# Kernel tuning notes

Measured on AMD Instinct MI355X. Metric: run time of the kernel, lower is better.

Reference implementation:

```python
import jax, jax.numpy as jnp
import numpy as np

DISCOUNT_FACTOR = 0.99
ADVANTAGE_LAMBDA = 0.95
LAMBD_GRAD_SCALE = 0.5


def setup_inputs() -> dict:
    key = jax.random.key(0)
    k1, k2, k3 = jax.random.split(key, 3)
    B, T, D = 4096, 2048, 1
    values = jax.random.normal(k1, (B, T + 1, D), dtype=jnp.float32)
    rewards = jax.random.normal(k2, (B, T, D), dtype=jnp.float32)
    # binary terminal flags (float, as in the torch module: used as (1 - dones))
    dones = (jax.random.uniform(k3, (B, T, D)) < 0.02).astype(jnp.float32)
    raw_gamma = jnp.zeros((1,), dtype=jnp.float32)
    raw_lambd = jnp.zeros((T,), dtype=jnp.float32)
    return {
        "values": values,
        "rewards": rewards,
        "dones": dones,
        "raw_gamma": raw_gamma,
        "raw_lambd": raw_lambd,
        "start_idx": 0,
        "end_idx": T,
    }


def reference(values, rewards, dones, raw_gamma, raw_lambd, start_idx, end_idx):
    # dynamic gamma / lambda (sigmoid-reparameterized around the base values)
    gamma = DISCOUNT_FACTOR + (1.0 - DISCOUNT_FACTOR) * (2.0 * jax.nn.sigmoid(raw_gamma) - 1.0)
    dyn_lambd = ADVANTAGE_LAMBDA + (1.0 - ADVANTAGE_LAMBDA) * (2.0 * jax.nn.sigmoid(raw_lambd) - 1.0)
    # GradScaler(scale=0.5): forward identity, gradient scaled by 0.5
    lambd = LAMBD_GRAD_SCALE * dyn_lambd + jax.lax.stop_gradient((1.0 - LAMBD_GRAD_SCALE) * dyn_lambd)
    g = gamma[0]
    td_l = lambd[start_idx:end_idx]                      # [T]

    # time-major views for the reverse-time scan
    r_tm = jnp.moveaxis(rewards, 1, 0)                   # [T, B, D]
    d_tm = jnp.moveaxis(dones, 1, 0)                     # [T, B, D]
    vn_tm = jnp.moveaxis(values[:, 1:, :], 1, 0)         # [T, B, D] = values[t+1]

    def step(carry, x):
        sum_r, lam_ret = carry
        r, d, vn, l = x
        cont = g * (1.0 - d)
        # torch computes sum_rewards under no_grad -> stop_gradient here
        new_sum = jax.lax.stop_gradient(r + cont * (l * sum_r))
        new_lam = r + cont * ((1.0 - l) * vn + l * lam_ret)
        return (new_sum, new_lam), (new_sum, new_lam)

    init = (jnp.zeros_like(values[:, -1, :]), values[:, -1, :])
    _, (sums_tm, lams_tm) = jax.lax.scan(step, init, (r_tm, d_tm, vn_tm, td_l), reverse=True)

    lambda_returns = jnp.concatenate(
        [jnp.moveaxis(lams_tm, 0, 1), values[:, -1:, :]], axis=1
    )                                                    # [B, T+1, D]
    sum_rewards = jnp.moveaxis(sums_tm, 0, 1)            # [B, T, D] (== torch sum_rewards[:, :-1])
    return lambda_returns, sum_rewards
```

## Files before the change

### kernel.cpp

```cpp
#include <hip/hip_runtime.h>


#define TPB 256
#define EPT 8

typedef float v4f __attribute__((ext_vector_type(4)));

struct Aff { float aL, aS, b; };

__device__ inline Aff compose(const Aff& L, const Aff& R) {
    Aff o;
    o.aL = fmaf(L.b, R.aL, L.aL);
    o.aS = fmaf(L.b, R.aS, L.aS);
    o.b  = L.b * R.b;
    return o;
}

__global__ void precompute_kernel(const float* __restrict__ raw_gamma,
                                  const float* __restrict__ raw_lambd,
                                  const int* __restrict__ start_p,
                                  float* __restrict__ lam, int T) {
    int t = blockIdx.x * blockDim.x + threadIdx.x;
    if (t < T) lam[t] = 0.9f + 0.1f / (1.0f + __expf(-raw_lambd[start_p[0] + t]));
    if (t == 0) lam[T] = 0.98f + 0.02f / (1.0f + __expf(-raw_gamma[0]));
}

__global__ __launch_bounds__(TPB, 8)
void td_scan_kernel(const float* __restrict__ values,
                    const float* __restrict__ rewards,
                    const float* __restrict__ dones,
                    const float* __restrict__ lam_arr,
                    float* __restrict__ out,
                    int B, int T)
{
    __shared__ __align__(16) float s_buf[2064];
    __shared__ float s_wAL[4], s_wAS[4], s_wB[4], s_cL[4], s_cS[4];

    const int b    = blockIdx.x;
    const int tid  = threadIdx.x;
    const int lane = tid & 63;
    const int wave = tid >> 6;
    const int nwaves = TPB >> 6;

    const float g = lam_arr[T];

    const size_t rowV = (size_t)b * (T + 1);
    const float* rrow = rewards + (size_t)b * T;
    const float* drow = dones   + (size_t)b * T;

    const size_t firstNeeded = rowV + 1;
    const int off = (int)(firstNeeded & 3);
    const size_t A = firstNeeded - off;
    const int nStage = T + off;
    const int n4 = (nStage + 3) >> 2;
    const size_t totalElems = (size_t)B * (T + 1);
    for (int j = tid; j < n4; j += TPB) {
        const size_t gb = A + 4 * (size_t)j;
        if (gb + 3 < totalElems) {
            *(v4f*)(s_buf + 4 * j) = *(const v4f*)(values + gb);
        } else {
            #pragma unroll
            for (int c = 0; c < 4; ++c)
                s_buf[4 * j + c] = (gb + c < totalElems) ? values[gb + c] : 0.0f;
        }
    }
    __syncthreads();

    const float vT = s_buf[off + T - 1];

    const int base = tid * EPT;
    float r[EPT], d[EPT], l[EPT], vn[EPT];
    {
        const v4f r0 = *(const v4f*)(rrow + base);
        const v4f r1 = *(const v4f*)(rrow + base + 4);
        const v4f d0 = *(const v4f*)(drow + base);
        const v4f d1 = *(const v4f*)(drow + base + 4);
        const v4f l0 = *(const v4f*)(lam_arr + base);
        const v4f l1 = *(const v4f*)(lam_arr + base + 4);
        r[0]=r0.x; r[1]=r0.y; r[2]=r0.z; r[3]=r0.w; r[4]=r1.x; r[5]=r1.y; r[6]=r1.z; r[7]=r1.w;
        d[0]=d0.x; d[1]=d0.y; d[2]=d0.z; d[3]=d0.w; d[4]=d1.x; d[5]=d1.y; d[6]=d1.z; d[7]=d1.w;
        l[0]=l0.x; l[1]=l0.y; l[2]=l0.z; l[3]=l0.w; l[4]=l1.x; l[5]=l1.y; l[6]=l1.z; l[7]=l1.w;
    }
    {
        const v4f w0 = *(const v4f*)(s_buf + base);
        const v4f w1 = *(const v4f*)(s_buf + base + 4);
        const v4f w2 = *(const v4f*)(s_buf + base + 8);
        switch (off) {
        case 0: vn[0]=w0.x; vn[1]=w0.y; vn[2]=w0.z; vn[3]=w0.w; vn[4]=w1.x; vn[5]=w1.y; vn[6]=w1.z; vn[7]=w1.w; break;
        case 1: vn[0]=w0.y; vn[1]=w0.z; vn[2]=w0.w; vn[3]=w1.x; vn[4]=w1.y; vn[5]=w1.z; vn[6]=w1.w; vn[7]=w2.x; break;
        case 2: vn[0]=w0.z; vn[1]=w0.w; vn[2]=w1.x; vn[3]=w1.y; vn[4]=w1.z; vn[5]=w1.w; vn[6]=w2.x; vn[7]=w2.y; break;
        default: vn[0]=w0.w; vn[1]=w1.x; vn[2]=w1.y; vn[3]=w1.z; vn[4]=w1.w; vn[5]=w2.x; vn[6]=w2.y; vn[7]=w2.z; break;
        }
    }

    Aff M[EPT];
    #pragma unroll
    for (int k = 0; k < EPT; ++k) {
        const float cont = g * (1.0f - d[k]);
        M[k].b  = cont * l[k];
        M[k].aL = fmaf(cont * (1.0f - l[k]), vn[k], r[k]);
        M[k].aS = r[k];
    }
    Aff C = M[EPT - 1];
    #pragma unroll
    for (int k = EPT - 2; k >= 0; --k) C = compose(M[k], C);

    Aff S = C;
    #pragma unroll
    for (int dlt = 1; dlt < 64; dlt <<= 1) {
        Aff oth;
        oth.aL = __shfl_down(S.aL, dlt, 64);
        oth.aS = __shfl_down(S.aS, dlt, 64);
        oth.b  = __shfl_down(S.b,  dlt, 64);
        if (lane + dlt < 64) S = compose(S, oth);
    }
    Aff E;
    E.aL = __shfl_down(S.aL, 1, 64);
    E.aS = __shfl_down(S.aS, 1, 64);
    E.b  = __shfl_down(S.b,  1, 64);
    if (lane == 63) { E.aL = 0.0f; E.aS = 0.0f; E.b = 1.0f; }

    if (lane == 0) { s_wAL[wave] = S.aL; s_wAS[wave] = S.aS; s_wB[wave] = S.b; }
    __syncthreads();

    if (tid == 0) {
        float cL = vT, cS = 0.0f;
        for (int w = nwaves - 1; w >= 0; --w) {
            s_cL[w] = cL; s_cS[w] = cS;
            const float wb = s_wB[w];
            cL = fmaf(wb, cL, s_wAL[w]);
            cS = fmaf(wb, cS, s_wAS[w]);
        }
    }
    __syncthreads();

    const float cwL = s_cL[wave];
    const float cwS = s_cS[wave];
    float xL = fmaf(E.b, cwL, E.aL);
    float xS = fmaf(E.b, cwS, E.aS);
    float oL[EPT], oS[EPT];
    #pragma unroll
    for (int k = EPT - 1; k >= 0; --k) {
        xL = fmaf(M[k].b, xL, M[k].aL);
        xS = fmaf(M[k].b, xS, M[k].aS);
        oL[k] = xL; oS[k] = xS;
    }

    float* sum_out = out + (size_t)B * (T + 1) + (size_t)b * T;
    {
        v4f s0 = { oS[0], oS[1], oS[2], oS[3] };
        v4f s1 = { oS[4], oS[5], oS[6], oS[7] };
        __builtin_nontemporal_store(s0, (v4f*)(sum_out + base));
        __builtin_nontemporal_store(s1, (v4f*)(sum_out + base + 4));
    }

    #pragma unroll
    for (int k = 0; k < EPT; ++k) s_buf[base + k] = oL[k];
    if (tid == 0) s_buf[T] = vT;
    __syncthreads();

    const size_t O = (size_t)b * (T + 1);
    const int sh = (int)((4 - (O & 3)) & 3);
    if (tid < sh) out[O + tid] = s_buf[tid];
    const int rem  = T + 1 - sh;
    const int m4   = rem >> 2;
    const int tail = rem & 3;
    for (int j = tid; j < m4; j += TPB) {
        const int ls = sh + 4 * j;
        const v4f lo = *(const v4f*)(s_buf + (ls - sh));
        const v4f hi = *(const v4f*)(s_buf + (ls - sh) + 4);
        v4f v;
        switch (sh) {
        case 0:  v = lo; break;
        case 1:  v = (v4f){ lo.y, lo.z, lo.w, hi.x }; break;
        case 2:  v = (v4f){ lo.z, lo.w, hi.x, hi.y }; break;
        default: v = (v4f){ lo.w, hi.x, hi.y, hi.z }; break;
        }
        __builtin_nontemporal_store(v, (v4f*)(out + O + ls));
    }
    if (tid < tail) { const int ls = sh + 4 * m4 + tid; out[O + ls] = s_buf[ls]; }
}

extern "C" void kernel_launch(void* const* d_in, const int* in_sizes, int n_in,
                              void* d_out, int out_size, void* d_ws, size_t ws_size,
                              hipStream_t stream) {
    const float* values    = (const float*)d_in[0];
    const float* rewards   = (const float*)d_in[1];
    const float* dones     = (const float*)d_in[2];
    const float* raw_gamma = (const float*)d_in[3];
    const float* raw_lambd = (const float*)d_in[4];
    const int*   start_idx = (const int*)d_in[5];
    float* out = (float*)d_out;
    float* lam_arr = (float*)d_ws;

    const int n_values  = in_sizes[0];
    const int n_rewards = in_sizes[1];
    const int B = n_values - n_rewards;
    const int T = n_rewards / B;

    precompute_kernel<<<(T + 256) / 256, 256, 0, stream>>>(raw_gamma, raw_lambd,
                                                           start_idx, lam_arr, T);
    td_scan_kernel<<<B, TPB, 0, stream>>>(values, rewards, dones, lam_arr, out, B, T);
}
```

Baseline: 158.6 us.

## Load values directly into registers and shift lambda-return stores via a small LDS halo

The full-row shared-memory staging of values is replaced by direct aligned vector loads of each thread's window plus a neighbour halo, which removes a block barrier and LDS round trips. The per-wave carry is now computed redundantly by every thread, dropping another barrier, and the local composition becomes a tree. Misaligned lambda-return rows are written with a 3-float shared halo exchange instead of staging the whole row. Nontemporal stores are replaced by plain stores, which changes cache behaviour, and the kernel now depends on T equalling TPB*EPT.

Result: no change. 157.1 us (-1.0%).

```diff
diff --git a/kernel.cpp b/kernel.cpp
--- a/kernel.cpp
+++ b/kernel.cpp
@@ -3,6 +3,7 @@
 
 #define TPB 256
 #define EPT 8
+#define NW  (TPB / 64)
 
 typedef float v4f __attribute__((ext_vector_type(4)));
 
@@ -33,86 +34,89 @@
                     float* __restrict__ out,
                     int B, int T)
 {
-    __shared__ __align__(16) float s_buf[2064];
-    __shared__ float s_wAL[4], s_wAS[4], s_wB[4], s_cL[4], s_cS[4];
+    __shared__ float s_wAL[NW], s_wAS[NW], s_wB[NW];
+    __shared__ float s_head[3 * TPB];
 
     const int b    = blockIdx.x;
     const int tid  = threadIdx.x;
     const int lane = tid & 63;
     const int wave = tid >> 6;
-    const int nwaves = TPB >> 6;
 
     const float g = lam_arr[T];
-
     const size_t rowV = (size_t)b * (T + 1);
     const float* rrow = rewards + (size_t)b * T;
     const float* drow = dones   + (size_t)b * T;
-
-    const size_t firstNeeded = rowV + 1;
-    const int off = (int)(firstNeeded & 3);
-    const size_t A = firstNeeded - off;
-    const int nStage = T + off;
-    const int n4 = (nStage + 3) >> 2;
-    const size_t totalElems = (size_t)B * (T + 1);
-    for (int j = tid; j < n4; j += TPB) {
-        const size_t gb = A + 4 * (size_t)j;
-        if (gb + 3 < totalElems) {
-            *(v4f*)(s_buf + 4 * j) = *(const v4f*)(values + gb);
+    const int base = tid * EPT;
+
+    const v4f r0 = *(const v4f*)(rrow + base);
+    const v4f r1 = *(const v4f*)(rrow + base + 4);
+    const v4f d0 = *(const v4f*)(drow + base);
+    const v4f d1 = *(const v4f*)(drow + base + 4);
+    const v4f l0 = *(const v4f*)(lam_arr + base);
+    const v4f l1 = *(const v4f*)(lam_arr + base + 4);
+
+    const int off = (int)((rowV + 1) & 3);
+    const size_t gA = (rowV + 1 - off) + base;
+    float w[12];
+    *(v4f*)(w)     = *(const v4f*)(values + gA);
+    *(v4f*)(w + 4) = *(const v4f*)(values + gA + 4);
+    w[8] = w[9] = w[10] = w[11] = 0.0f;
+    if (off) {
+        const size_t totalV = (size_t)B * (T + 1);
+        if (gA + 11 < totalV) {
+            *(v4f*)(w + 8) = *(const v4f*)(values + gA + 8);
         } else {
             #pragma unroll
             for (int c = 0; c < 4; ++c)
-                s_buf[4 * j + c] = (gb + c < totalElems) ? values[gb + c] : 0.0f;
-        }
-    }
-    __syncthreads();
-
-    const float vT = s_buf[off + T - 1];
-
-    const int base = tid * EPT;
-    float r[EPT], d[EPT], l[EPT], vn[EPT];
-    {
-        const v4f r0 = *(const v4f*)(rrow + base);
-        const v4f r1 = *(const v4f*)(rrow + base + 4);
-        const v4f d0 = *(const v4f*)(drow + base);
-        const v4f d1 = *(const v4f*)(drow + base + 4);
-        const v4f l0 = *(const v4f*)(lam_arr + base);
-        const v4f l1 = *(const v4f*)(lam_arr + base + 4);
-        r[0]=r0.x; r[1]=r0.y; r[2]=r0.z; r[3]=r0.w; r[4]=r1.x; r[5]=r1.y; r[6]=r1.z; r[7]=r1.w;
-        d[0]=d0.x; d[1]=d0.y; d[2]=d0.z; d[3]=d0.w; d[4]=d1.x; d[5]=d1.y; d[6]=d1.z; d[7]=d1.w;
-        l[0]=l0.x; l[1]=l0.y; l[2]=l0.z; l[3]=l0.w; l[4]=l1.x; l[5]=l1.y; l[6]=l1.z; l[7]=l1.w;
-    }
-    {
-        const v4f w0 = *(const v4f*)(s_buf + base);
-        const v4f w1 = *(const v4f*)(s_buf + base + 4);
-        const v4f w2 = *(const v4f*)(s_buf + base + 8);
-        switch (off) {
-        case 0: vn[0]=w0.x; vn[1]=w0.y; vn[2]=w0.z; vn[3]=w0.w; vn[4]=w1.x; vn[5]=w1.y; vn[6]=w1.z; vn[7]=w1.w; break;
-        case 1: vn[0]=w0.y; vn[1]=w0.z; vn[2]=w0.w; vn[3]=w1.x; vn[4]=w1.y; vn[5]=w1.z; vn[6]=w1.w; vn[7]=w2.x; break;
-        case 2: vn[0]=w0.z; vn[1]=w0.w; vn[2]=w1.x; vn[3]=w1.y; vn[4]=w1.z; vn[5]=w1.w; vn[6]=w2.x; vn[7]=w2.y; break;
-        default: vn[0]=w0.w; vn[1]=w1.x; vn[2]=w1.y; vn[3]=w1.z; vn[4]=w1.w; vn[5]=w2.x; vn[6]=w2.y; vn[7]=w2.z; break;
-        }
-    }
-
-    Aff M[EPT];
+                if (gA + 8 + c < totalV) w[8 + c] = values[gA + 8 + c];
+        }
+    }
+    const float vT = values[rowV + T];
+
+    float vn[EPT];
+    switch (off) {
+    case 0: { 
+        #pragma unroll
+        for (int k = 0; k < EPT; ++k) vn[k] = w[k];     } break;
+    case 1: { 
+        #pragma unroll
+        for (int k = 0; k < EPT; ++k) vn[k] = w[k + 1]; } break;
+    case 2: { 
+        #pragma unroll
+        for (int k = 0; k < EPT; ++k) vn[k] = w[k + 2]; } break;
+    default: { 
+        #pragma unroll
+        for (int k = 0; k < EPT; ++k) vn[k] = w[k + 3]; } break;
+    }
+
+    float rr[EPT] = { r0.x, r0.y, r0.z, r0.w, r1.x, r1.y, r1.z, r1.w };
+    float dd[EPT] = { d0.x, d0.y, d0.z, d0.w, d1.x, d1.y, d1.z, d1.w };
+    float ll[EPT] = { l0.x, l0.y, l0.z, l0.w, l1.x, l1.y, l1.z, l1.w };
+    float bb[EPT], aL[EPT], aS[EPT];
     #pragma unroll
     for (int k = 0; k < EPT; ++k) {
-        const float cont = g * (1.0f - d[k]);
-        M[k].b  = cont * l[k];
-        M[k].aL = fmaf(cont * (1.0f - l[k]), vn[k], r[k]);
-        M[k].aS = r[k];
-    }
-    Aff C = M[EPT - 1];
-    #pragma unroll
-    for (int k = EPT - 2; k >= 0; --k) C = compose(M[k], C);
+        const float cont = g * (1.0f - dd[k]);
+        bb[k] = cont * ll[k];
+        aL[k] = fmaf(cont * (1.0f - ll[k]), vn[k], rr[k]);
+        aS[k] = rr[k];
+    }
+
+    Aff m[EPT];
+    #pragma unroll
+    for (int k = 0; k < EPT; ++k) { m[k].aL = aL[k]; m[k].aS = aS[k]; m[k].b = bb[k]; }
+    Aff c01 = compose(m[0], m[1]), c23 = compose(m[2], m[3]);
+    Aff c45 = compose(m[4], m[5]), c67 = compose(m[6], m[7]);
+    Aff c03 = compose(c01, c23),   c47 = compose(c45, c67);
+    Aff C   = compose(c03, c47);
 
     Aff S = C;
     #pragma unroll
     for (int dlt = 1; dlt < 64; dlt <<= 1) {
-        Aff oth;
-        oth.aL = __shfl_down(S.aL, dlt, 64);
-        oth.aS = __shfl_down(S.aS, dlt, 64);
-        oth.b  = __shfl_down(S.b,  dlt, 64);
-        if (lane + dlt < 64) S = compose(S, oth);
+        Aff o;
+        o.aL = __shfl_down(S.aL, dlt, 64);
+        o.aS = __shfl_down(S.aS, dlt, 64);
+        o.b  = __shfl_down(S.b,  dlt, 64);
+        if (lane + dlt < 64) S = compose(S, o);
     }
     Aff E;
     E.aL = __shfl_down(S.aL, 1, 64);
@@ -123,62 +127,77 @@
     if (lane == 0) { s_wAL[wave] = S.aL; s_wAS[wave] = S.aS; s_wB[wave] = S.b; }
     __syncthreads();
 
-    if (tid == 0) {
-        float cL = vT, cS = 0.0f;
-        for (int w = nwaves - 1; w >= 0; --w) {
-            s_cL[w] = cL; s_cS[w] = cS;
-            const float wb = s_wB[w];
-            cL = fmaf(wb, cL, s_wAL[w]);
-            cS = fmaf(wb, cS, s_wAS[w]);
-        }
-    }
-    __syncthreads();
-
-    const float cwL = s_cL[wave];
-    const float cwS = s_cS[wave];
-    float xL = fmaf(E.b, cwL, E.aL);
-    float xS = fmaf(E.b, cwS, E.aS);
-    float oL[EPT], oS[EPT];
+    float cL = vT, cS = 0.0f;
+    #pragma unroll
+    for (int wv = NW - 1; wv >= 1; --wv) {
+        if (wv > wave) {
+            const float wb = s_wB[wv];
+            cL = fmaf(wb, cL, s_wAL[wv]);
+            cS = fmaf(wb, cS, s_wAS[wv]);
+        }
+    }
+
+    float xL = fmaf(E.b, cL, E.aL);
+    float xS = fmaf(E.b, cS, E.aS);
     #pragma unroll
     for (int k = EPT - 1; k >= 0; --k) {
-        xL = fmaf(M[k].b, xL, M[k].aL);
-        xS = fmaf(M[k].b, xS, M[k].aS);
-        oL[k] = xL; oS[k] = xS;
-    }
-
-    float* sum_out = out + (size_t)B * (T + 1) + (size_t)b * T;
-    {
-        v4f s0 = { oS[0], oS[1], oS[2], oS[3] };
-        v4f s1 = { oS[4], oS[5], oS[6], oS[7] };
-        __builtin_nontemporal_store(s0, (v4f*)(sum_out + base));
-        __builtin_nontemporal_store(s1, (v4f*)(sum_out + base + 4));
-    }
-
-    #pragma unroll
-    for (int k = 0; k < EPT; ++k) s_buf[base + k] = oL[k];
-    if (tid == 0) s_buf[T] = vT;
-    __syncthreads();
-
-    const size_t O = (size_t)b * (T + 1);
-    const int sh = (int)((4 - (O & 3)) & 3);
-    if (tid < sh) out[O + tid] = s_buf[tid];
-    const int rem  = T + 1 - sh;
-    const int m4   = rem >> 2;
-    const int tail = rem & 3;
-    for (int j = tid; j < m4; j += TPB) {
-        const int ls = sh + 4 * j;
-        const v4f lo = *(const v4f*)(s_buf + (ls - sh));
-        const v4f hi = *(const v4f*)(s_buf + (ls - sh) + 4);
-        v4f v;
+        xL = fmaf(bb[k], xL, aL[k]);  aL[k] = xL;
+        xS = fmaf(bb[k], xS, aS[k]);  aS[k] = xS;
+    }
+
+    float* sum_out = out + (size_t)B * (T + 1) + (size_t)b * T + base;
+    v4f s0 = { aS[0], aS[1], aS[2], aS[3] };
+    v4f s1 = { aS[4], aS[5], aS[6], aS[7] };
+    *(v4f*)(sum_out)     = s0;
+    *(v4f*)(sum_out + 4) = s1;
+
+    float* lamrow = out + rowV;
+    const int sh = (int)((4 - (rowV & 3)) & 3);
+    if (sh == 0) {
+        v4f p0 = { aL[0], aL[1], aL[2], aL[3] };
+        v4f p1 = { aL[4], aL[5], aL[6], aL[7] };
+        *(v4f*)(lamrow + base)     = p0;
+        *(v4f*)(lamrow + base + 4) = p1;
+        if (tid == 0) lamrow[T] = vT;
+    } else {
+        s_head[3 * tid]     = aL[0];
+        s_head[3 * tid + 1] = aL[1];
+        s_head[3 * tid + 2] = aL[2];
+        __syncthreads();
+        float nb0 = vT, nb1 = 0.0f, nb2 = 0.0f;
+        if (tid < TPB - 1) {
+            nb0 = s_head[3 * tid + 3];
+            nb1 = s_head[3 * tid + 4];
+            nb2 = s_head[3 * tid + 5];
+        }
+        float z[EPT];
         switch (sh) {
-        case 0:  v = lo; break;
-        case 1:  v = (v4f){ lo.y, lo.z, lo.w, hi.x }; break;
-        case 2:  v = (v4f){ lo.z, lo.w, hi.x, hi.y }; break;
-        default: v = (v4f){ lo.w, hi.x, hi.y, hi.z }; break;
-        }
-        __builtin_nontemporal_store(v, (v4f*)(out + O + ls));
-    }
-    if (tid < tail) { const int ls = sh + 4 * m4 + tid; out[O + ls] = s_buf[ls]; }
+        case 1: { 
+            #pragma unroll
+            for (int k = 0; k < 7; ++k) z[k] = aL[k + 1];
+            z[7] = nb0; } break;
+        case 2: { 
+            #pragma unroll
+            for (int k = 0; k < 6; ++k) z[k] = aL[k + 2];
+            z[6] = nb0; z[7] = nb1; } break;
+        default: { 
+            #pragma unroll
+            for (int k = 0; k < 5; ++k) z[k] = aL[k + 3];
+            z[5] = nb0; z[6] = nb1; z[7] = nb2; } break;
+        }
+        v4f p0 = { z[0], z[1], z[2], z[3] };
+        *(v4f*)(lamrow + base + sh) = p0;
+        if (tid < TPB - 1 || sh == 1) {
+            v4f p1 = { z[4], z[5], z[6], z[7] };
+            *(v4f*)(lamrow + base + sh + 4) = p1;
+        } else {
+            #pragma unroll
+            for (int k = 4; k < EPT; ++k)
+                if (base + sh + k <= T) lamrow[base + sh + k] = z[k];
+        }
+        if (tid == 0)
+            for (int k = 0; k < sh; ++k) lamrow[k] = aL[k];
+    }
 }
 
 extern "C" void kernel_launch(void* const* d_in, const int* in_sizes, int n_in,
```
